# Kernel optimization log

Hardware: AMD Instinct MI355X
Metric: run time of the kernel (lower is better)

## Reference

```python
import jax, jax.numpy as jnp
import numpy as np


def setup_inputs() -> dict:
    key = jax.random.key(0)
    k1, k2 = jax.random.split(key)
    center = jax.random.normal(k1, (4096,), dtype=jnp.float32)
    error = jax.random.normal(k2, (8192, 4096), dtype=jnp.float32) * 0.01
    return {"center": center, "error": error}


def reference(center, error):
    # Zonotope ReLU abstract transformer.
    center_orig_shape = center.shape
    error_orig_shape = error.shape
    c = center.reshape(-1)                      # (d,)
    e = error.reshape(error.shape[0], -1)       # (n_error, d)
    n_error, d = e.shape

    apt = jnp.sum(jnp.abs(e), axis=0)           # (d,) interval radius
    ub = c + apt
    lb = c - apt

    cross = (ub > 0) & (lb < 0)                 # unstable neurons
    act = lb >= 0                               # stably active
    # dead (ub <= 0): slope = 0, mu = 0 -> center/error zeroed

    denom = jnp.where(cross, ub - lb, jnp.float32(1.0))
    slope = jnp.where(cross, ub / denom, jnp.float32(0.0))
    mu = jnp.where(cross, -slope * lb * jnp.float32(0.5), jnp.float32(0.0))

    new_center = jnp.where(act, c, slope * c + mu)          # (d,)
    col_scale = jnp.where(act, jnp.float32(1.0), slope)     # (d,)
    top = e * col_scale[None, :]                             # (n_error, d)
    # One fresh error term per crossing neuron; padded to d rows (diagonal),
    # zero rows where the neuron is not crossing (static output shape).
    bottom = jnp.diag(mu)                                    # (d, d)
    new_error = jnp.concatenate([top, bottom], axis=0)       # (n_error + d, d)

    new_center = new_center.reshape(center_orig_shape)
    new_error = new_error.reshape((n_error + d,) + error_orig_shape[1:])
    return new_center, new_error
```

## Files before the change

### kernel.cpp

```cpp
#include <hip/hip_runtime.h>

#define D       4096
#define NERR    8192
#define DF4     (D / 4)
#define NSTRIP  128
#define SF4     (DF4 / NSTRIP)
#define TPB     1024
#define RPP     (TPB / SF4)
#define NPASS   (NERR / RPP)

typedef float f32x4 __attribute__((ext_vector_type(4)));

__global__ __launch_bounds__(TPB) void k_fused(const f32x4* __restrict__ e4,
                                               const f32x4* __restrict__ c4,
                                               f32x4* __restrict__ out_center4,
                                               f32x4* __restrict__ top4,
                                               f32x4* __restrict__ bot4) {
    __shared__ f32x4 red[TPB];
    __shared__ f32x4 scl[SF4];

    const int t   = threadIdx.x;
    const int bid = blockIdx.x;

    if (bid < NSTRIP) {
        const int s   = bid;
        const int cf  = t & (SF4 - 1);
        const int r0  = t >> 3;
        const int off = s * SF4 + cf;

        f32x4 acc = (f32x4)(0.f, 0.f, 0.f, 0.f);
        #pragma unroll 8
        for (int k = 0; k < NPASS; ++k) {
            const int r = r0 + k * RPP;
            f32x4 v = e4[(size_t)r * DF4 + off];
            acc.x += fabsf(v.x);
            acc.y += fabsf(v.y);
            acc.z += fabsf(v.z);
            acc.w += fabsf(v.w);
        }
        red[t] = acc;
        __syncthreads();
        #pragma unroll
        for (int step = 64; step >= 1; step >>= 1) {
            if (r0 < step) red[t] += red[t + step * SF4];
            __syncthreads();
        }

        if (t < SF4) {
            const int g  = s * SF4 + t;
            const f32x4 apt = red[t];
            const f32x4 cen = c4[g];
            f32x4 oc, cs;
            #pragma unroll
            for (int j = 0; j < 4; ++j) {
                const float c  = cen[j];
                const float ub = c + apt[j];
                const float lb = c - apt[j];
                const bool cross = (ub > 0.f) && (lb < 0.f);
                const bool act   = (lb >= 0.f);
                const float denom = cross ? (ub - lb) : 1.f;
                const float slope = cross ? (ub / denom) : 0.f;
                const float mu    = cross ? (-slope * lb * 0.5f) : 0.f;
                oc[j] = act ? c : (slope * c + mu);
                cs[j] = act ? 1.f : slope;
                f32x4 dv = (f32x4)(0.f, 0.f, 0.f, 0.f);
                dv[j] = mu;
                __builtin_nontemporal_store(dv, &bot4[(size_t)(4 * g + j) * DF4 + g]);
            }
            out_center4[g] = oc;
            scl[t] = cs;
        }
        __syncthreads();

        const f32x4 cs = scl[cf];
        #pragma unroll 8
        for (int k = 0; k < NPASS; ++k) {
            const int r = r0 + k * RPP;
            f32x4 v = e4[(size_t)r * DF4 + off];
            v *= cs;
            __builtin_nontemporal_store(v, &top4[(size_t)r * DF4 + off]);
        }
    } else {
        const int fb   = bid - NSTRIP;
        const int row0 = fb * 32;
        const f32x4 z = (f32x4)(0.f, 0.f, 0.f, 0.f);
        #pragma unroll 4
        for (int j = 0; j < 32; ++j) {
            const int row = row0 + j;
            const int dg  = row >> 2;
            if (t != dg)
                __builtin_nontemporal_store(z, &bot4[(size_t)row * DF4 + t]);
        }
    }
}

extern "C" void kernel_launch(void* const* d_in, const int* in_sizes, int n_in,
                              void* d_out, int out_size, void* d_ws, size_t ws_size,
                              hipStream_t stream) {
    const float* center = (const float*)d_in[0];
    const float* error  = (const float*)d_in[1];
    float* out = (float*)d_out;

    float* out_center = out;
    float* out_top    = out + D;
    float* out_bottom = out + (size_t)D + (size_t)NERR * D;

    k_fused<<<2 * NSTRIP, TPB, 0, stream>>>(
        (const f32x4*)error, (const f32x4*)center,
        (f32x4*)out_center, (f32x4*)out_top, (f32x4*)out_bottom);
}
```

Measured before the change: 82.72 us.

## Split columns into 256 narrow strips, shuffle reduction, fold zero-fill into every block

Each block now owns a 16-column strip (4 float4s) instead of 32, so all 256 blocks do the reduce-and-scale work and none are dedicated only to zero-filling. The LDS tree reduction with many barriers is replaced by wavefront xor-shuffles plus one small cross-wave sum. Each block also writes 16 rows of the zero diagonal block. Block IDs are remapped so neighbouring strips land on different XCDs. Narrower strips mean each wave touches 64-byte row segments across many rows, which may reduce coalescing and DRAM burst efficiency.

```diff
diff --git a/kernel.cpp b/kernel.cpp
--- a/kernel.cpp
+++ b/kernel.cpp
@@ -1,96 +1,98 @@
 #include <hip/hip_runtime.h>
 
-#define D       4096
-#define NERR    8192
-#define DF4     (D / 4)
-#define NSTRIP  128
-#define SF4     (DF4 / NSTRIP)
-#define TPB     1024
-#define RPP     (TPB / SF4)
-#define NPASS   (NERR / RPP)
+#define D     4096
+#define NERR  8192
+#define DF4   (D / 4)
+#define NBLK  256
+#define SF4   4
+#define TPB   1024
+#define RPP   (TPB / SF4)
+#define NPASS (NERR / RPP)
+#define NWAVE (TPB / 64)
 
 typedef float f32x4 __attribute__((ext_vector_type(4)));
 
 __global__ __launch_bounds__(TPB) void k_fused(const f32x4* __restrict__ e4,
                                                const f32x4* __restrict__ c4,
-                                               f32x4* __restrict__ out_center4,
+                                               f32x4* __restrict__ oc4,
                                                f32x4* __restrict__ top4,
                                                f32x4* __restrict__ bot4) {
-    __shared__ f32x4 red[TPB];
+    __shared__ f32x4 wred[NWAVE * SF4];
     __shared__ f32x4 scl[SF4];
 
-    const int t   = threadIdx.x;
-    const int bid = blockIdx.x;
+    const int t    = threadIdx.x;
+    const int lane = t & 63;
+    const int w    = t >> 6;
+    const int cf   = t & (SF4 - 1);
+    const int r0   = t >> 2;
+    const int s    = (blockIdx.x & 7) * 32 + (blockIdx.x >> 3);
+    const int off  = s * SF4 + cf;
 
-    if (bid < NSTRIP) {
-        const int s   = bid;
-        const int cf  = t & (SF4 - 1);
-        const int r0  = t >> 3;
-        const int off = s * SF4 + cf;
+    f32x4 acc = (f32x4)(0.f, 0.f, 0.f, 0.f);
+    #pragma unroll 8
+    for (int k = 0; k < NPASS; ++k) {
+        f32x4 v = e4[(size_t)(k * RPP + r0) * DF4 + off];
+        acc.x += fabsf(v.x);
+        acc.y += fabsf(v.y);
+        acc.z += fabsf(v.z);
+        acc.w += fabsf(v.w);
+    }
+    #pragma unroll
+    for (int st = 4; st <= 32; st <<= 1) {
+        acc.x += __shfl_xor(acc.x, st, 64);
+        acc.y += __shfl_xor(acc.y, st, 64);
+        acc.z += __shfl_xor(acc.z, st, 64);
+        acc.w += __shfl_xor(acc.w, st, 64);
+    }
+    if (lane < SF4) wred[w * SF4 + lane] = acc;
+    __syncthreads();
 
-        f32x4 acc = (f32x4)(0.f, 0.f, 0.f, 0.f);
-        #pragma unroll 8
-        for (int k = 0; k < NPASS; ++k) {
-            const int r = r0 + k * RPP;
-            f32x4 v = e4[(size_t)r * DF4 + off];
-            acc.x += fabsf(v.x);
-            acc.y += fabsf(v.y);
-            acc.z += fabsf(v.z);
-            acc.w += fabsf(v.w);
+    if (t < SF4) {
+        f32x4 apt = wred[t];
+        #pragma unroll
+        for (int w2 = 1; w2 < NWAVE; ++w2) apt += wred[w2 * SF4 + t];
+        const int g = s * SF4 + t;
+        const f32x4 cen = c4[g];
+        f32x4 oc, cs;
+        #pragma unroll
+        for (int j = 0; j < 4; ++j) {
+            const float c  = cen[j];
+            const float ub = c + apt[j];
+            const float lb = c - apt[j];
+            const bool cross = (ub > 0.f) && (lb < 0.f);
+            const bool act   = (lb >= 0.f);
+            const float denom = cross ? (ub - lb) : 1.f;
+            const float slope = cross ? (ub / denom) : 0.f;
+            const float mu    = cross ? (-slope * lb * 0.5f) : 0.f;
+            oc[j] = act ? c : (slope * c + mu);
+            cs[j] = act ? 1.f : slope;
+            f32x4 dv = (f32x4)(0.f, 0.f, 0.f, 0.f);
+            dv[j] = mu;
+            __builtin_nontemporal_store(dv, &bot4[(size_t)(4 * g + j) * DF4 + g]);
         }
-        red[t] = acc;
-        __syncthreads();
-        #pragma unroll
-        for (int step = 64; step >= 1; step >>= 1) {
-            if (r0 < step) red[t] += red[t + step * SF4];
-            __syncthreads();
-        }
+        oc4[g] = oc;
+        scl[t] = cs;
+    }
+    __syncthreads();
 
-        if (t < SF4) {
-            const int g  = s * SF4 + t;
-            const f32x4 apt = red[t];
-            const f32x4 cen = c4[g];
-            f32x4 oc, cs;
-            #pragma unroll
-            for (int j = 0; j < 4; ++j) {
-                const float c  = cen[j];
-                const float ub = c + apt[j];
-                const float lb = c - apt[j];
-                const bool cross = (ub > 0.f) && (lb < 0.f);
-                const bool act   = (lb >= 0.f);
-                const float denom = cross ? (ub - lb) : 1.f;
-                const float slope = cross ? (ub / denom) : 0.f;
-                const float mu    = cross ? (-slope * lb * 0.5f) : 0.f;
-                oc[j] = act ? c : (slope * c + mu);
-                cs[j] = act ? 1.f : slope;
-                f32x4 dv = (f32x4)(0.f, 0.f, 0.f, 0.f);
-                dv[j] = mu;
-                __builtin_nontemporal_store(dv, &bot4[(size_t)(4 * g + j) * DF4 + g]);
-            }
-            out_center4[g] = oc;
-            scl[t] = cs;
-        }
-        __syncthreads();
+    const f32x4 cs = scl[cf];
+    #pragma unroll 8
+    for (int k = 0; k < NPASS; ++k) {
+        const size_t idx = (size_t)(k * RPP + r0) * DF4 + off;
+        f32x4 v = e4[idx];
+        v *= cs;
+        __builtin_nontemporal_store(v, &top4[idx]);
+    }
 
-        const f32x4 cs = scl[cf];
-        #pragma unroll 8
-        for (int k = 0; k < NPASS; ++k) {
-            const int r = r0 + k * RPP;
-            f32x4 v = e4[(size_t)r * DF4 + off];
-            v *= cs;
-            __builtin_nontemporal_store(v, &top4[(size_t)r * DF4 + off]);
-        }
-    } else {
-        const int fb   = bid - NSTRIP;
-        const int row0 = fb * 32;
-        const f32x4 z = (f32x4)(0.f, 0.f, 0.f, 0.f);
-        #pragma unroll 4
-        for (int j = 0; j < 32; ++j) {
-            const int row = row0 + j;
-            const int dg  = row >> 2;
-            if (t != dg)
-                __builtin_nontemporal_store(z, &bot4[(size_t)row * DF4 + t]);
-        }
+    const int r  = 16 * s + (t >> 6);
+    const int c0 = t & 63;
+    const int dg = r >> 2;
+    const f32x4 z = (f32x4)(0.f, 0.f, 0.f, 0.f);
+    #pragma unroll
+    for (int j = 0; j < 16; ++j) {
+        const int c = c0 + j * 64;
+        if (c != dg)
+            __builtin_nontemporal_store(z, &bot4[(size_t)r * DF4 + c]);
     }
 }
 
@@ -105,7 +107,7 @@
     float* out_top    = out + D;
     float* out_bottom = out + (size_t)D + (size_t)NERR * D;
 
-    k_fused<<<2 * NSTRIP, TPB, 0, stream>>>(
+    k_fused<<<NBLK, TPB, 0, stream>>>(
         (const f32x4*)error, (const f32x4*)center,
         (f32x4*)out_center, (f32x4*)out_top, (f32x4*)out_bottom);
 }
```

Result: slower. 92.55 us (+11.9%).
